# Performance work log

Hardware: AMD Instinct MI355X
Metric: run time of the kernel (lower is better)

Reference implementation:

```python
import jax, jax.numpy as jnp
import numpy as np

N, E, F_IN, HID, L_EXTRA, G = 50000, 800000, 128, 128, 3, 256

def gcn_conv(x, W, b, src, dst, norm):
    # PyG GCNConv: out = D^-1/2 (A+I) D^-1/2 (X W) + b  (self-loops included in src/dst)
    xw = x @ W                                  # [N, out]
    msg = xw[src] * norm[:, None]               # [E+N, out]
    return jax.ops.segment_sum(msg, dst, num_segments=N) + b

def setup_inputs() -> dict:
    key = jax.random.key(0)
    ks = jax.random.split(key, 12)
    x = jax.random.normal(ks[0], (N, F_IN), dtype=jnp.float32)
    edge_index = jax.random.randint(ks[1], (2, E), 0, N, dtype=jnp.int64)
    batch = jnp.sort(jax.random.randint(ks[2], (N,), 0, G, dtype=jnp.int64))
    s = 1.0 / np.sqrt(HID)
    W0 = jax.random.uniform(ks[3], (F_IN, HID), jnp.float32, -s, s)
    b0 = jnp.zeros((HID,), jnp.float32)
    Wh = jax.random.uniform(ks[4], (L_EXTRA, HID, HID), jnp.float32, -s, s)
    bh = jnp.zeros((L_EXTRA, HID), jnp.float32)
    s1 = 1.0 / np.sqrt(3 * HID)
    lin1_w = jax.random.uniform(ks[5], (3 * HID, HID), jnp.float32, -s1, s1)
    lin1_b = jax.random.uniform(ks[6], (HID,), jnp.float32, -s1, s1)
    s2 = 1.0 / np.sqrt(HID)
    lin2_w = jax.random.uniform(ks[7], (HID, 2), jnp.float32, -s2, s2)
    lin2_b = jax.random.uniform(ks[8], (2,), jnp.float32, -s2, s2)
    return {"x": x, "edge_index": edge_index, "batch": batch,
            "W0": W0, "b0": b0, "Wh": Wh, "bh": bh,
            "lin1_w": lin1_w, "lin1_b": lin1_b, "lin2_w": lin2_w, "lin2_b": lin2_b}

def reference(x, edge_index, batch, W0, b0, Wh, bh, lin1_w, lin1_b, lin2_w, lin2_b):
    # add self-loops once (shared by all layers)
    loop = jnp.arange(N, dtype=edge_index.dtype)
    src = jnp.concatenate([edge_index[0], loop])
    dst = jnp.concatenate([edge_index[1], loop])
    deg = jax.ops.segment_sum(jnp.ones_like(dst, dtype=x.dtype), dst, num_segments=N)
    dinv = jnp.where(deg > 0, jax.lax.rsqrt(deg), 0.0)
    norm = dinv[src] * dinv[dst]                # [E+N]

    h = jax.nn.relu(gcn_conv(x, W0, b0, src, dst, norm))
    for i in range(L_EXTRA):
        h = jax.nn.relu(gcn_conv(h, Wh[i], bh[i], src, dst, norm))

    # multi-pool over graphs in the batch
    p_sum = jax.ops.segment_sum(h, batch, num_segments=G)
    cnt = jax.ops.segment_sum(jnp.ones((N,), h.dtype), batch, num_segments=G)
    p_mean = p_sum / jnp.maximum(cnt, 1.0)[:, None]
    p_max = jax.ops.segment_max(h, batch, num_segments=G)
    p_max = jnp.where(jnp.isfinite(p_max), p_max, 0.0)  # guard empty graphs
    g = jnp.concatenate([p_sum, p_mean, p_max], axis=1)  # [G, 3*HID]

    g = jax.nn.relu(g @ lin1_w + lin1_b)        # dropout p=0.5 is identity in eval
    logits = g @ lin2_w + lin2_b
    return jax.nn.log_softmax(logits, axis=-1)
```

## Files before the change

kernel.cpp:

```cpp
#include <hip/hip_runtime.h>
#include <hip/hip_fp16.h>
#include <cstddef>

typedef _Float16 f16x8 __attribute__((ext_vector_type(8)));
typedef float f32x4 __attribute__((ext_vector_type(4)));
typedef unsigned short ushort8 __attribute__((ext_vector_type(8)));


__global__ __launch_bounds__(256) void k_bhist(const int* __restrict__ dst, int* __restrict__ bcnt, int e) {
    __shared__ int lh[256];
    int t = threadIdx.x;
    lh[t] = 0;
    __syncthreads();
    for (int i = blockIdx.x * 256 + t; i < e; i += gridDim.x * 256)
        atomicAdd(&lh[dst[i] >> 8], 1);
    __syncthreads();
    if (lh[t] > 0) atomicAdd(&bcnt[t], lh[t]);
}

__global__ __launch_bounds__(256) void k_bscan(const int* __restrict__ bcnt, int* __restrict__ bebase,
                                               int* __restrict__ bcbase, int* __restrict__ bcur,
                                               int* __restrict__ rowptr, int nbk, int n, int e) {
    __shared__ int se[256], sc[256];
    int t = threadIdx.x;
    int ec = (t < nbk) ? bcnt[t] : 0;
    int nodes = 0;
    if (t < nbk) {
        nodes = n - t * 256;
        if (nodes > 256) nodes = 256;
        if (nodes < 0) nodes = 0;
    }
    se[t] = ec;
    sc[t] = ec + nodes;
    __syncthreads();
    for (int off = 1; off < 256; off <<= 1) {
        int ve = (t >= off) ? se[t - off] : 0;
        int vc = (t >= off) ? sc[t - off] : 0;
        __syncthreads();
        se[t] += ve;
        sc[t] += vc;
        __syncthreads();
    }
    if (t < nbk) {
        bebase[t] = se[t] - ec;
        bcbase[t] = sc[t] - (ec + nodes);
        bcur[t]   = se[t] - ec;
    }
    if (t == 0) {
        bebase[nbk] = e;
        rowptr[n] = e + n;
    }
}

__global__ __launch_bounds__(256) void k_bscatter(const int* __restrict__ src, const int* __restrict__ dst,
                                                  int* __restrict__ bcur, int* __restrict__ bedges, int e) {
    __shared__ int lh[256];
    __shared__ int gbase[256];
    int t = threadIdx.x;
    lh[t] = 0;
    __syncthreads();
    int base = blockIdx.x * 4096;
    int s_[16], d_[16];
#pragma unroll
    for (int u = 0; u < 16; ++u) {
        int j = base + u * 256 + t;
        if (j < e) {
            s_[u] = src[j];
            d_[u] = dst[j];
            atomicAdd(&lh[d_[u] >> 8], 1);
        } else {
            d_[u] = -1;
        }
    }
    __syncthreads();
    if (lh[t] > 0) gbase[t] = atomicAdd(&bcur[t], lh[t]);
    __syncthreads();
    lh[t] = 0;
    __syncthreads();
#pragma unroll
    for (int u = 0; u < 16; ++u) {
        if (d_[u] >= 0) {
            int bk = d_[u] >> 8;
            int lpos = atomicAdd(&lh[bk], 1);
            bedges[gbase[bk] + lpos] = (s_[u] << 8) | (d_[u] & 255);
        }
    }
}

__global__ __launch_bounds__(256) void k_bcsr(const int* __restrict__ bedges, const int* __restrict__ bebase,
                                              const int* __restrict__ bcbase, int* __restrict__ rowptr,
                                              float* __restrict__ dinv, int* __restrict__ csr_s, int n) {
    __shared__ int lh[256], lcur[256];
    int b = blockIdx.x, t = threadIdx.x;
    int n0 = b << 8;
    int nb = n - n0; if (nb > 256) nb = 256;
    int e0 = bebase[b], e1 = bebase[b + 1];
    int cb = bcbase[b];
    lh[t] = 0;
    __syncthreads();
    for (int i = e0 + t; i < e1; i += 256)
        atomicAdd(&lh[bedges[i] & 255], 1);
    __syncthreads();
    int deg = (t < nb) ? (lh[t] + 1) : 0;
    __syncthreads();
    lh[t] = deg;
    __syncthreads();
    for (int off = 1; off < 256; off <<= 1) {
        int v = (t >= off) ? lh[t - off] : 0;
        __syncthreads();
        lh[t] += v;
        __syncthreads();
    }
    int lrp = lh[t] - deg;
    if (t < nb) {
        rowptr[n0 + t] = cb + lrp;
        dinv[n0 + t] = rsqrtf((float)deg);
    }
    lcur[t] = lrp;
    __syncthreads();
    for (int i = e0 + t; i < e1; i += 256) {
        int ed = bedges[i];
        int pos = cb + atomicAdd(&lcur[ed & 255], 1);
        csr_s[pos] = (int)((unsigned)ed >> 8);
    }
    if (t < nb) {
        int pos = cb + atomicAdd(&lcur[t], 1);
        csr_s[pos] = n0 + t;
    }
}

__global__ __launch_bounds__(256) void k_wprep(const float* __restrict__ W0, const float* __restrict__ Wh,
                                               __half* __restrict__ WP, int* __restrict__ bcnt, int nlayers) {
    int layer = blockIdx.x;
    int t = threadIdx.x;
    if (layer >= nlayers) {
        bcnt[t] = 0;
        return;
    }
    const float* W = (layer == 0) ? W0 : Wh + (size_t)(layer - 1) * 16384;
    __half* out = WP + (size_t)layer * 16384;
    for (int u = 0; u < 64; ++u) {
        int o = u * 256 + t;
        int i  = o & 7;
        int l  = (o >> 3) & 63;
        int kc = (o >> 9) & 3;
        int nt = o >> 11;
        int k   = kc * 32 + ((l >> 4) << 3) + i;
        int col = nt * 16 + (l & 15);
        out[o] = __float2half(W[k * 128 + col]);
    }
}

__global__ __launch_bounds__(256) void k_gemm(const __half* __restrict__ H, const __half* __restrict__ WP,
                                              const float* __restrict__ dinv, __half* __restrict__ O,
                                              int n) {
    __shared__ __half wl[16384];
    const int t = threadIdx.x;
#pragma unroll
    for (int u = 0; u < 8; ++u) {
        int idx = (u * 256 + t) * 8;
        *(ushort8*)&wl[idx] = *(const ushort8*)&WP[idx];
    }
    const int wid = t >> 6, l = t & 63;
    const int row0 = blockIdx.x * 128 + wid * 32;
    const int ar = l & 15, g = l >> 4;

    f16x8 a[2][4];
    float dv[2][4];
#pragma unroll
    for (int mt = 0; mt < 2; ++mt) {
        int row = row0 + mt * 16 + ar;
        int rc = min(row, n - 1);
#pragma unroll
        for (int kc = 0; kc < 4; ++kc)
            a[mt][kc] = *(const f16x8*)&H[(size_t)rc * 128 + kc * 32 + g * 8];
#pragma unroll
        for (int r = 0; r < 4; ++r) {
            int orow = row0 + mt * 16 + g * 4 + r;
            dv[mt][r] = dinv[min(orow, n - 1)];
        }
    }
    __syncthreads();

#pragma unroll
    for (int nt = 0; nt < 8; ++nt) {
        f16x8 b[4];
#pragma unroll
        for (int kc = 0; kc < 4; ++kc)
            b[kc] = *(f16x8*)&wl[((nt * 4 + kc) * 64 + l) * 8];
#pragma unroll
        for (int mt = 0; mt < 2; ++mt) {
            f32x4 acc = {0.f, 0.f, 0.f, 0.f};
#pragma unroll
            for (int kc = 0; kc < 4; ++kc)
                acc = __builtin_amdgcn_mfma_f32_16x16x32_f16(a[mt][kc], b[kc], acc, 0, 0, 0);
#pragma unroll
            for (int r = 0; r < 4; ++r) {
                int orow = row0 + mt * 16 + g * 4 + r;
                if (orow < n)
                    O[(size_t)orow * 128 + nt * 16 + ar] = __float2half(acc[r] * dv[mt][r]);
            }
        }
    }
}

__global__ __launch_bounds__(256) void k_gemm32(const float* __restrict__ H, const __half* __restrict__ WP,
                                                const float* __restrict__ dinv, __half* __restrict__ O,
                                                int n) {
    __shared__ __half wl[16384];
    const int t = threadIdx.x;
#pragma unroll
    for (int u = 0; u < 8; ++u) {
        int idx = (u * 256 + t) * 8;
        *(ushort8*)&wl[idx] = *(const ushort8*)&WP[idx];
    }
    const int wid = t >> 6, l = t & 63;
    const int row0 = blockIdx.x * 128 + wid * 32;
    const int ar = l & 15, g = l >> 4;

    f16x8 a[2][4];
    float dv[2][4];
#pragma unroll
    for (int mt = 0; mt < 2; ++mt) {
        int row = row0 + mt * 16 + ar;
        int rc = min(row, n - 1);
#pragma unroll
        for (int kc = 0; kc < 4; ++kc) {
            float4 p0 = *(const float4*)&H[(size_t)rc * 128 + kc * 32 + g * 8];
            float4 p1 = *(const float4*)&H[(size_t)rc * 128 + kc * 32 + g * 8 + 4];
            f16x8 av;
            av[0] = (_Float16)p0.x; av[1] = (_Float16)p0.y; av[2] = (_Float16)p0.z; av[3] = (_Float16)p0.w;
            av[4] = (_Float16)p1.x; av[5] = (_Float16)p1.y; av[6] = (_Float16)p1.z; av[7] = (_Float16)p1.w;
            a[mt][kc] = av;
        }
#pragma unroll
        for (int r = 0; r < 4; ++r) {
            int orow = row0 + mt * 16 + g * 4 + r;
            dv[mt][r] = dinv[min(orow, n - 1)];
        }
    }
    __syncthreads();

#pragma unroll
    for (int nt = 0; nt < 8; ++nt) {
        f16x8 b[4];
#pragma unroll
        for (int kc = 0; kc < 4; ++kc)
            b[kc] = *(f16x8*)&wl[((nt * 4 + kc) * 64 + l) * 8];
#pragma unroll
        for (int mt = 0; mt < 2; ++mt) {
            f32x4 acc = {0.f, 0.f, 0.f, 0.f};
#pragma unroll
            for (int kc = 0; kc < 4; ++kc)
                acc = __builtin_amdgcn_mfma_f32_16x16x32_f16(a[mt][kc], b[kc], acc, 0, 0, 0);
#pragma unroll
            for (int r = 0; r < 4; ++r) {
                int orow = row0 + mt * 16 + g * 4 + r;
                if (orow < n)
                    O[(size_t)orow * 128 + nt * 16 + ar] = __float2half(acc[r] * dv[mt][r]);
            }
        }
    }
}

__global__ __launch_bounds__(256) void k_agg(const __half* __restrict__ XW, const int* __restrict__ cs,
                                             const int* __restrict__ rp, const float* __restrict__ dinv,
                                             const float* __restrict__ bias, __half* __restrict__ Hn, int n) {
    int wid  = (blockIdx.x * 256 + threadIdx.x) >> 6;
    int lane = threadIdx.x & 63;
    if (wid >= n) return;
    int s = rp[wid], e = rp[wid + 1];
    const int g = lane >> 4, fs = lane & 15;
    float acc0[8], acc1[8];
#pragma unroll
    for (int k = 0; k < 8; ++k) { acc0[k] = 0.f; acc1[k] = 0.f; }
    for (int base = s; base < e; base += 64) {
        int m = e - base;
        if (m > 64) m = 64;
        int myi = (lane < m) ? cs[base + lane] : 0;
#pragma unroll 2
        for (int j = 0; j < m; j += 8) {
            int ia = __shfl(myi, j + g);
            int ib = __shfl(myi, j + 4 + g);
            if (j + g < m) {
                f16x8 va = *(const f16x8*)&XW[(size_t)ia * 128 + fs * 8];
#pragma unroll
                for (int k = 0; k < 8; ++k) acc0[k] += (float)va[k];
            }
            if (j + 4 + g < m) {
                f16x8 vb = *(const f16x8*)&XW[(size_t)ib * 128 + fs * 8];
#pragma unroll
                for (int k = 0; k < 8; ++k) acc1[k] += (float)vb[k];
            }
        }
    }
#pragma unroll
    for (int k = 0; k < 8; ++k) acc0[k] += acc1[k];
#pragma unroll
    for (int k = 0; k < 8; ++k) acc0[k] += __shfl_xor(acc0[k], 16);
#pragma unroll
    for (int k = 0; k < 8; ++k) acc0[k] += __shfl_xor(acc0[k], 32);
    if (g == 0) {
        float dvv = dinv[wid];
        float4 bb0 = *(const float4*)&bias[fs * 8];
        float4 bb1 = *(const float4*)&bias[fs * 8 + 4];
        float bb[8] = {bb0.x, bb0.y, bb0.z, bb0.w, bb1.x, bb1.y, bb1.z, bb1.w};
        f16x8 o;
#pragma unroll
        for (int k = 0; k < 8; ++k)
            o[k] = (_Float16)fmaxf(fmaf(acc0[k], dvv, bb[k]), 0.f);
        *(f16x8*)&Hn[(size_t)wid * 128 + fs * 8] = o;
    }
}

__global__ __launch_bounds__(256) void k_poolhead(const __half* __restrict__ H, const int* __restrict__ batch,
                                                  const float* __restrict__ w1, const float* __restrict__ b1,
                                                  const float* __restrict__ w2, const float* __restrict__ b2,
                                                  float* __restrict__ out, int n) {
    __shared__ float lsum[16][128];
    __shared__ float lmax[16][128];
    __shared__ float gv[384];
    __shared__ float o1[128];
    __shared__ int bnd[2];
    int g = blockIdx.x, t = threadIdx.x;
    if (t < 2) {
        int key = g + t;
        int lo = 0, hi = n;
        while (lo < hi) {
            int mid = (lo + hi) >> 1;
            if (batch[mid] < key) lo = mid + 1; else hi = mid;
        }
        bnd[t] = lo;
    }
    __syncthreads();
    const int s = bnd[0], e = bnd[1];
    const int rg = t >> 4, fb = t & 15;
    float sum8[8], max8[8];
#pragma unroll
    for (int j = 0; j < 8; ++j) { sum8[j] = 0.f; max8[j] = 0.f; }
    for (int r = s + rg; r < e; r += 16) {
        f16x8 v = *(const f16x8*)&H[(size_t)r * 128 + fb * 8];
#pragma unroll
        for (int j = 0; j < 8; ++j) {
            float x = (float)v[j];
            sum8[j] += x;
            max8[j] = fmaxf(max8[j], x);
        }
    }
#pragma unroll
    for (int j = 0; j < 8; ++j) {
        lsum[rg][fb * 8 + j] = sum8[j];
        lmax[rg][fb * 8 + j] = max8[j];
    }
    __syncthreads();
    if (t < 128) {
        float sum = 0.f, mx = 0.f;
#pragma unroll
        for (int r = 0; r < 16; ++r) {
            sum += lsum[r][t];
            mx = fmaxf(mx, lmax[r][t]);
        }
        float cnt = (float)(e - s);
        gv[t]       = sum;
        gv[128 + t] = sum / fmaxf(cnt, 1.f);
        gv[256 + t] = mx;
    }
    __syncthreads();
    if (t < 128) {
        float acc = b1[t];
#pragma unroll 8
        for (int k = 0; k < 384; ++k) acc = fmaf(gv[k], w1[k * 128 + t], acc);
        o1[t] = fmaxf(acc, 0.f);
    }
    __syncthreads();
    if (t < 64) {
        float p0 = o1[t] * w2[t * 2 + 0] + o1[t + 64] * w2[(t + 64) * 2 + 0];
        float p1 = o1[t] * w2[t * 2 + 1] + o1[t + 64] * w2[(t + 64) * 2 + 1];
        for (int off = 32; off > 0; off >>= 1) {
            p0 += __shfl_down(p0, off);
            p1 += __shfl_down(p1, off);
        }
        if (t == 0) {
            float l0 = p0 + b2[0], l1 = p1 + b2[1];
            float m = fmaxf(l0, l1);
            float lse = m + logf(expf(l0 - m) + expf(l1 - m));
            out[g * 2 + 0] = l0 - lse;
            out[g * 2 + 1] = l1 - lse;
        }
    }
}


extern "C" void kernel_launch(void* const* d_in, const int* in_sizes, int n_in,
                              void* d_out, int out_size, void* d_ws, size_t ws_size,
                              hipStream_t stream) {
    const float* x     = (const float*)d_in[0];
    const int*   ei    = (const int*)d_in[1];
    const int*   batch = (const int*)d_in[2];
    const float* W0    = (const float*)d_in[3];
    const float* b0    = (const float*)d_in[4];
    const float* Wh    = (const float*)d_in[5];
    const float* bh    = (const float*)d_in[6];
    const float* l1w   = (const float*)d_in[7];
    const float* l1b   = (const float*)d_in[8];
    const float* l2w   = (const float*)d_in[9];
    const float* l2b   = (const float*)d_in[10];
    float* out = (float*)d_out;

    const int N  = in_sizes[0] / 128;
    const int E  = in_sizes[1] / 2;
    const int G  = out_size / 2;
    const int LX = in_sizes[5] / (128 * 128);
    const int NB = (N + 255) / 256;

    const int* src = ei;
    const int* dst = ei + E;

    char* p = (char*)d_ws;
    auto alloc = [&](size_t bytes) -> void* {
        void* r = (void*)p;
        p += (bytes + 255) & ~(size_t)255;
        return r;
    };
    int*    rowptr = (int*)alloc((size_t)(N + 1) * 4);
    float*  dinv   = (float*)alloc((size_t)N * 4);
    int*    bcnt   = (int*)alloc(1040);
    int*    bebase = (int*)alloc(1040);
    int*    bcbase = (int*)alloc(1040);
    int*    bcur   = (int*)alloc(1040);
    int*    csr_s  = (int*)alloc((size_t)(E + N) * 4);
    int*    bedges = (int*)alloc((size_t)E * 4);
    __half* h16    = (__half*)alloc((size_t)N * 128 * 2);
    __half* xw16   = (__half*)alloc((size_t)N * 128 * 2);
    __half* wp     = (__half*)alloc((size_t)(LX + 1) * 16384 * 2);

    k_wprep<<<LX + 2, 256, 0, stream>>>(W0, Wh, wp, bcnt, LX + 1);

    k_bhist<<<NB, 256, 0, stream>>>(dst, bcnt, E);
    k_bscan<<<1, 256, 0, stream>>>(bcnt, bebase, bcbase, bcur, rowptr, NB, N, E);
    k_bscatter<<<(E + 4095) / 4096, 256, 0, stream>>>(src, dst, bcur, bedges, E);
    k_bcsr<<<NB, 256, 0, stream>>>(bedges, bebase, bcbase, rowptr, dinv, csr_s, N);

    const int gemmBlocks = (N + 127) / 128;
    const int aggBlocks  = (N + 3) / 4;

    k_gemm32<<<gemmBlocks, 256, 0, stream>>>(x, wp, dinv, xw16, N);
    k_agg<<<aggBlocks, 256, 0, stream>>>(xw16, csr_s, rowptr, dinv, b0, h16, N);
    for (int l = 0; l < LX; ++l) {
        k_gemm<<<gemmBlocks, 256, 0, stream>>>(h16, wp + (size_t)(l + 1) * 16384, dinv, xw16, N);
        k_agg<<<aggBlocks, 256, 0, stream>>>(xw16, csr_s, rowptr, dinv, bh + (size_t)l * 128, h16, N);
    }

    k_poolhead<<<G, 256, 0, stream>>>(h16, batch, l1w, l1b, l2w, l2b, out, N);
}
```

Baseline: 249.5 us.

## Store features in four 32-column planes and aggregate per plane for cache locality

Feature matrices move from row-major [N,128] to four planar [N,32] chunks, and the aggregation kernel now runs a separate block range per chunk. Each chunk of the gathered table is about 3.2 MB, so the random neighbour gathers in one pass should stay in L2 instead of sweeping the full 12.8 MB table. The cost is four times as many waves, each rereading the CSR indices and rowptr, plus 64-byte gather segments instead of 256-byte rows. The GEMM and pooling kernels are updated to read and write the planar layout.

```diff
diff --git a/kernel.cpp b/kernel.cpp
--- a/kernel.cpp
+++ b/kernel.cpp
@@ -164,6 +164,7 @@
     const int wid = t >> 6, l = t & 63;
     const int row0 = blockIdx.x * 128 + wid * 32;
     const int ar = l & 15, g = l >> 4;
+    const size_t pn = (size_t)n * 32;
 
     f16x8 a[2][4];
     float dv[2][4];
@@ -173,7 +174,7 @@
         int rc = min(row, n - 1);
 #pragma unroll
         for (int kc = 0; kc < 4; ++kc)
-            a[mt][kc] = *(const f16x8*)&H[(size_t)rc * 128 + kc * 32 + g * 8];
+            a[mt][kc] = *(const f16x8*)&H[pn * kc + (size_t)rc * 32 + g * 8];
 #pragma unroll
         for (int r = 0; r < 4; ++r) {
             int orow = row0 + mt * 16 + g * 4 + r;
@@ -198,7 +199,8 @@
             for (int r = 0; r < 4; ++r) {
                 int orow = row0 + mt * 16 + g * 4 + r;
                 if (orow < n)
-                    O[(size_t)orow * 128 + nt * 16 + ar] = __float2half(acc[r] * dv[mt][r]);
+                    O[pn * (nt >> 1) + (size_t)orow * 32 + (nt & 1) * 16 + ar] =
+                        __float2half(acc[r] * dv[mt][r]);
             }
         }
     }
@@ -217,6 +219,7 @@
     const int wid = t >> 6, l = t & 63;
     const int row0 = blockIdx.x * 128 + wid * 32;
     const int ar = l & 15, g = l >> 4;
+    const size_t pn = (size_t)n * 32;
 
     f16x8 a[2][4];
     float dv[2][4];
@@ -257,59 +260,62 @@
             for (int r = 0; r < 4; ++r) {
                 int orow = row0 + mt * 16 + g * 4 + r;
                 if (orow < n)
-                    O[(size_t)orow * 128 + nt * 16 + ar] = __float2half(acc[r] * dv[mt][r]);
+                    O[pn * (nt >> 1) + (size_t)orow * 32 + (nt & 1) * 16 + ar] =
+                        __float2half(acc[r] * dv[mt][r]);
             }
         }
     }
 }
 
-__global__ __launch_bounds__(256) void k_agg(const __half* __restrict__ XW, const int* __restrict__ cs,
-                                             const int* __restrict__ rp, const float* __restrict__ dinv,
-                                             const float* __restrict__ bias, __half* __restrict__ Hn, int n) {
-    int wid  = (blockIdx.x * 256 + threadIdx.x) >> 6;
+__global__ __launch_bounds__(256) void k_aggc(const __half* __restrict__ XWp, const int* __restrict__ cs,
+                                              const int* __restrict__ rp, const float* __restrict__ dinv,
+                                              const float* __restrict__ bias, __half* __restrict__ Hp,
+                                              int n, int bpc) {
+    int c   = blockIdx.x / bpc;
+    int nb  = blockIdx.x - c * bpc;
+    int wid = (nb * 256 + threadIdx.x) >> 6;
     int lane = threadIdx.x & 63;
     if (wid >= n) return;
+    const size_t pn = (size_t)n * 32;
+    const __half* P = XWp + pn * c;
     int s = rp[wid], e = rp[wid + 1];
-    const int g = lane >> 4, fs = lane & 15;
-    float acc0[8], acc1[8];
-#pragma unroll
-    for (int k = 0; k < 8; ++k) { acc0[k] = 0.f; acc1[k] = 0.f; }
+    const int g4 = lane >> 2, q = lane & 3;
+    float acc[8];
+#pragma unroll
+    for (int k = 0; k < 8; ++k) acc[k] = 0.f;
     for (int base = s; base < e; base += 64) {
         int m = e - base;
         if (m > 64) m = 64;
         int myi = (lane < m) ? cs[base + lane] : 0;
 #pragma unroll 2
-        for (int j = 0; j < m; j += 8) {
-            int ia = __shfl(myi, j + g);
-            int ib = __shfl(myi, j + 4 + g);
-            if (j + g < m) {
-                f16x8 va = *(const f16x8*)&XW[(size_t)ia * 128 + fs * 8];
-#pragma unroll
-                for (int k = 0; k < 8; ++k) acc0[k] += (float)va[k];
+        for (int j = 0; j < m; j += 16) {
+            int r = j + g4;
+            int idx = __shfl(myi, r);
+            if (r < m) {
+                f16x8 v = *(const f16x8*)&P[(size_t)idx * 32 + q * 8];
+#pragma unroll
+                for (int k = 0; k < 8; ++k) acc[k] += (float)v[k];
             }
-            if (j + 4 + g < m) {
-                f16x8 vb = *(const f16x8*)&XW[(size_t)ib * 128 + fs * 8];
-#pragma unroll
-                for (int k = 0; k < 8; ++k) acc1[k] += (float)vb[k];
-            }
-        }
-    }
-#pragma unroll
-    for (int k = 0; k < 8; ++k) acc0[k] += acc1[k];
-#pragma unroll
-    for (int k = 0; k < 8; ++k) acc0[k] += __shfl_xor(acc0[k], 16);
-#pragma unroll
-    for (int k = 0; k < 8; ++k) acc0[k] += __shfl_xor(acc0[k], 32);
-    if (g == 0) {
+        }
+    }
+#pragma unroll
+    for (int k = 0; k < 8; ++k) acc[k] += __shfl_xor(acc[k], 4);
+#pragma unroll
+    for (int k = 0; k < 8; ++k) acc[k] += __shfl_xor(acc[k], 8);
+#pragma unroll
+    for (int k = 0; k < 8; ++k) acc[k] += __shfl_xor(acc[k], 16);
+#pragma unroll
+    for (int k = 0; k < 8; ++k) acc[k] += __shfl_xor(acc[k], 32);
+    if (g4 == 0) {
         float dvv = dinv[wid];
-        float4 bb0 = *(const float4*)&bias[fs * 8];
-        float4 bb1 = *(const float4*)&bias[fs * 8 + 4];
+        float4 bb0 = *(const float4*)&bias[c * 32 + q * 8];
+        float4 bb1 = *(const float4*)&bias[c * 32 + q * 8 + 4];
         float bb[8] = {bb0.x, bb0.y, bb0.z, bb0.w, bb1.x, bb1.y, bb1.z, bb1.w};
         f16x8 o;
 #pragma unroll
         for (int k = 0; k < 8; ++k)
-            o[k] = (_Float16)fmaxf(fmaf(acc0[k], dvv, bb[k]), 0.f);
-        *(f16x8*)&Hn[(size_t)wid * 128 + fs * 8] = o;
+            o[k] = (_Float16)fmaxf(fmaf(acc[k], dvv, bb[k]), 0.f);
+        *(f16x8*)&Hp[pn * c + (size_t)wid * 32 + q * 8] = o;
     }
 }
 
@@ -335,11 +341,14 @@
     __syncthreads();
     const int s = bnd[0], e = bnd[1];
     const int rg = t >> 4, fb = t & 15;
+    const size_t pn = (size_t)n * 32;
+    const __half* Hc = H + pn * (fb >> 2);
+    const int fo = (fb & 3) * 8;
     float sum8[8], max8[8];
 #pragma unroll
     for (int j = 0; j < 8; ++j) { sum8[j] = 0.f; max8[j] = 0.f; }
     for (int r = s + rg; r < e; r += 16) {
-        f16x8 v = *(const f16x8*)&H[(size_t)r * 128 + fb * 8];
+        f16x8 v = *(const f16x8*)&Hc[(size_t)r * 32 + fo];
 #pragma unroll
         for (int j = 0; j < 8; ++j) {
             float x = (float)v[j];
@@ -442,13 +451,13 @@
     k_bcsr<<<NB, 256, 0, stream>>>(bedges, bebase, bcbase, rowptr, dinv, csr_s, N);
 
     const int gemmBlocks = (N + 127) / 128;
-    const int aggBlocks  = (N + 3) / 4;
+    const int bpc        = (N + 3) / 4;
 
     k_gemm32<<<gemmBlocks, 256, 0, stream>>>(x, wp, dinv, xw16, N);
-    k_agg<<<aggBlocks, 256, 0, stream>>>(xw16, csr_s, rowptr, dinv, b0, h16, N);
+    k_aggc<<<4 * bpc, 256, 0, stream>>>(xw16, csr_s, rowptr, dinv, b0, h16, N, bpc);
     for (int l = 0; l < LX; ++l) {
         k_gemm<<<gemmBlocks, 256, 0, stream>>>(h16, wp + (size_t)(l + 1) * 16384, dinv, xw16, N);
-        k_agg<<<aggBlocks, 256, 0, stream>>>(xw16, csr_s, rowptr, dinv, bh + (size_t)l * 128, h16, N);
+        k_aggc<<<4 * bpc, 256, 0, stream>>>(xw16, csr_s, rowptr, dinv, bh + (size_t)l * 128, h16, N, bpc);
     }
 
     k_poolhead<<<G, 256, 0, stream>>>(h16, batch, l1w, l1b, l2w, l2b, out, N);
```

Result: slower. 411.1 us (+64.8%).

## Merge setup kernels and overlap first-layer GEMM with CSR build

Applied to the files above, without the earlier changes.

Weight packing is folded into the degree-histogram kernel, and the bucket-to-CSR build shares one launch with the first-layer GEMM. Because that GEMM can no longer wait for dinv, it skips the source-side scaling, and the first aggregation applies dinv per gathered source row instead. The aggregation inner loop is also fully unrolled with an early break. This removes launches and lets independent work overlap, at the cost of an extra dinv gather per edge in layer one.

```diff
diff --git a/kernel.cpp b/kernel.cpp
--- a/kernel.cpp
+++ b/kernel.cpp
@@ -6,16 +6,35 @@
 typedef float f32x4 __attribute__((ext_vector_type(4)));
 typedef unsigned short ushort8 __attribute__((ext_vector_type(8)));
 
-
-__global__ __launch_bounds__(256) void k_bhist(const int* __restrict__ dst, int* __restrict__ bcnt, int e) {
+__global__ __launch_bounds__(256) void k_setup1(const float* __restrict__ W0, const float* __restrict__ Wh,
+                                                __half* __restrict__ WP, int nlayers,
+                                                const int* __restrict__ dst, int* __restrict__ bcnt,
+                                                int e, int nb) {
     __shared__ int lh[256];
     int t = threadIdx.x;
-    lh[t] = 0;
-    __syncthreads();
-    for (int i = blockIdx.x * 256 + t; i < e; i += gridDim.x * 256)
-        atomicAdd(&lh[dst[i] >> 8], 1);
-    __syncthreads();
-    if (lh[t] > 0) atomicAdd(&bcnt[t], lh[t]);
+    if ((int)blockIdx.x < nlayers) {
+        int layer = blockIdx.x;
+        const float* W = (layer == 0) ? W0 : Wh + (size_t)(layer - 1) * 16384;
+        __half* out = WP + (size_t)layer * 16384;
+        for (int u = 0; u < 64; ++u) {
+            int o = u * 256 + t;
+            int i  = o & 7;
+            int l  = (o >> 3) & 63;
+            int kc = (o >> 9) & 3;
+            int nt = o >> 11;
+            int k   = kc * 32 + ((l >> 4) << 3) + i;
+            int col = nt * 16 + (l & 15);
+            out[o] = __float2half(W[k * 128 + col]);
+        }
+    } else {
+        int bi = blockIdx.x - nlayers;
+        lh[t] = 0;
+        __syncthreads();
+        for (int i = bi * 256 + t; i < e; i += nb * 256)
+            atomicAdd(&lh[dst[i] >> 8], 1);
+        __syncthreads();
+        if (lh[t] > 0) atomicAdd(&bcnt[t], lh[t]);
+    }
 }
 
 __global__ __launch_bounds__(256) void k_bscan(const int* __restrict__ bcnt, int* __restrict__ bebase,
@@ -87,67 +106,100 @@
     }
 }
 
-__global__ __launch_bounds__(256) void k_bcsr(const int* __restrict__ bedges, const int* __restrict__ bebase,
-                                              const int* __restrict__ bcbase, int* __restrict__ rowptr,
-                                              float* __restrict__ dinv, int* __restrict__ csr_s, int n) {
-    __shared__ int lh[256], lcur[256];
-    int b = blockIdx.x, t = threadIdx.x;
-    int n0 = b << 8;
-    int nb = n - n0; if (nb > 256) nb = 256;
-    int e0 = bebase[b], e1 = bebase[b + 1];
-    int cb = bcbase[b];
-    lh[t] = 0;
-    __syncthreads();
-    for (int i = e0 + t; i < e1; i += 256)
-        atomicAdd(&lh[bedges[i] & 255], 1);
-    __syncthreads();
-    int deg = (t < nb) ? (lh[t] + 1) : 0;
-    __syncthreads();
-    lh[t] = deg;
-    __syncthreads();
-    for (int off = 1; off < 256; off <<= 1) {
-        int v = (t >= off) ? lh[t - off] : 0;
-        __syncthreads();
-        lh[t] += v;
-        __syncthreads();
-    }
-    int lrp = lh[t] - deg;
-    if (t < nb) {
-        rowptr[n0 + t] = cb + lrp;
-        dinv[n0 + t] = rsqrtf((float)deg);
-    }
-    lcur[t] = lrp;
-    __syncthreads();
-    for (int i = e0 + t; i < e1; i += 256) {
-        int ed = bedges[i];
-        int pos = cb + atomicAdd(&lcur[ed & 255], 1);
-        csr_s[pos] = (int)((unsigned)ed >> 8);
-    }
-    if (t < nb) {
-        int pos = cb + atomicAdd(&lcur[t], 1);
-        csr_s[pos] = n0 + t;
-    }
-}
-
-__global__ __launch_bounds__(256) void k_wprep(const float* __restrict__ W0, const float* __restrict__ Wh,
-                                               __half* __restrict__ WP, int* __restrict__ bcnt, int nlayers) {
-    int layer = blockIdx.x;
-    int t = threadIdx.x;
-    if (layer >= nlayers) {
-        bcnt[t] = 0;
-        return;
-    }
-    const float* W = (layer == 0) ? W0 : Wh + (size_t)(layer - 1) * 16384;
-    __half* out = WP + (size_t)layer * 16384;
-    for (int u = 0; u < 64; ++u) {
-        int o = u * 256 + t;
-        int i  = o & 7;
-        int l  = (o >> 3) & 63;
-        int kc = (o >> 9) & 3;
-        int nt = o >> 11;
-        int k   = kc * 32 + ((l >> 4) << 3) + i;
-        int col = nt * 16 + (l & 15);
-        out[o] = __float2half(W[k * 128 + col]);
+__global__ __launch_bounds__(256) void k_mix(const int* __restrict__ bedges, const int* __restrict__ bebase,
+                                             const int* __restrict__ bcbase, int* __restrict__ rowptr,
+                                             float* __restrict__ dinv, int* __restrict__ csr_s, int n,
+                                             const float* __restrict__ X, const __half* __restrict__ WP,
+                                             __half* __restrict__ O, int nbk) {
+    __shared__ __half wl[16384];
+    const int t = threadIdx.x;
+    if ((int)blockIdx.x < nbk) {
+        int* lh   = (int*)wl;
+        int* lcur = lh + 256;
+        int b = blockIdx.x;
+        int n0 = b << 8;
+        int nb = n - n0; if (nb > 256) nb = 256;
+        int e0 = bebase[b], e1 = bebase[b + 1];
+        int cb = bcbase[b];
+        lh[t] = 0;
+        __syncthreads();
+        for (int i = e0 + t; i < e1; i += 256)
+            atomicAdd(&lh[bedges[i] & 255], 1);
+        __syncthreads();
+        int deg = (t < nb) ? (lh[t] + 1) : 0;
+        __syncthreads();
+        lh[t] = deg;
+        __syncthreads();
+        for (int off = 1; off < 256; off <<= 1) {
+            int v = (t >= off) ? lh[t - off] : 0;
+            __syncthreads();
+            lh[t] += v;
+            __syncthreads();
+        }
+        int lrp = lh[t] - deg;
+        if (t < nb) {
+            rowptr[n0 + t] = cb + lrp;
+            dinv[n0 + t] = rsqrtf((float)deg);
+        }
+        lcur[t] = lrp;
+        __syncthreads();
+        for (int i = e0 + t; i < e1; i += 256) {
+            int ed = bedges[i];
+            int pos = cb + atomicAdd(&lcur[ed & 255], 1);
+            csr_s[pos] = (int)((unsigned)ed >> 8);
+        }
+        if (t < nb) {
+            int pos = cb + atomicAdd(&lcur[t], 1);
+            csr_s[pos] = n0 + t;
+        }
+    } else {
+#pragma unroll
+        for (int u = 0; u < 8; ++u) {
+            int idx = (u * 256 + t) * 8;
+            *(ushort8*)&wl[idx] = *(const ushort8*)&WP[idx];
+        }
+        const int gb = blockIdx.x - nbk;
+        const int wid = t >> 6, l = t & 63;
+        const int row0 = gb * 128 + wid * 32;
+        const int ar = l & 15, g = l >> 4;
+
+        f16x8 a[2][4];
+#pragma unroll
+        for (int mt = 0; mt < 2; ++mt) {
+            int row = row0 + mt * 16 + ar;
+            int rc = min(row, n - 1);
+#pragma unroll
+            for (int kc = 0; kc < 4; ++kc) {
+                float4 p0 = *(const float4*)&X[(size_t)rc * 128 + kc * 32 + g * 8];
+                float4 p1 = *(const float4*)&X[(size_t)rc * 128 + kc * 32 + g * 8 + 4];
+                f16x8 av;
+                av[0] = (_Float16)p0.x; av[1] = (_Float16)p0.y; av[2] = (_Float16)p0.z; av[3] = (_Float16)p0.w;
+                av[4] = (_Float16)p1.x; av[5] = (_Float16)p1.y; av[6] = (_Float16)p1.z; av[7] = (_Float16)p1.w;
+                a[mt][kc] = av;
+            }
+        }
+        __syncthreads();
+
+#pragma unroll
+        for (int nt = 0; nt < 8; ++nt) {
+            f16x8 b[4];
+#pragma unroll
+            for (int kc = 0; kc < 4; ++kc)
+                b[kc] = *(f16x8*)&wl[((nt * 4 + kc) * 64 + l) * 8];
+#pragma unroll
+            for (int mt = 0; mt < 2; ++mt) {
+                f32x4 acc = {0.f, 0.f, 0.f, 0.f};
+#pragma unroll
+                for (int kc = 0; kc < 4; ++kc)
+                    acc = __builtin_amdgcn_mfma_f32_16x16x32_f16(a[mt][kc], b[kc], acc, 0, 0, 0);
+#pragma unroll
+                for (int r = 0; r < 4; ++r) {
+                    int orow = row0 + mt * 16 + g * 4 + r;
+                    if (orow < n)
+                        O[(size_t)orow * 128 + nt * 16 + ar] = __float2half(acc[r]);
+                }
+            }
+        }
     }
 }
 
@@ -204,65 +256,7 @@
     }
 }
 
-__global__ __launch_bounds__(256) void k_gemm32(const float* __restrict__ H, const __half* __restrict__ WP,
-                                                const float* __restrict__ dinv, __half* __restrict__ O,
-                                                int n) {
-    __shared__ __half wl[16384];
-    const int t = threadIdx.x;
-#pragma unroll
-    for (int u = 0; u < 8; ++u) {
-        int idx = (u * 256 + t) * 8;
-        *(ushort8*)&wl[idx] = *(const ushort8*)&WP[idx];
-    }
-    const int wid = t >> 6, l = t & 63;
-    const int row0 = blockIdx.x * 128 + wid * 32;
-    const int ar = l & 15, g = l >> 4;
-
-    f16x8 a[2][4];
-    float dv[2][4];
-#pragma unroll
-    for (int mt = 0; mt < 2; ++mt) {
-        int row = row0 + mt * 16 + ar;
-        int rc = min(row, n - 1);
-#pragma unroll
-        for (int kc = 0; kc < 4; ++kc) {
-            float4 p0 = *(const float4*)&H[(size_t)rc * 128 + kc * 32 + g * 8];
-            float4 p1 = *(const float4*)&H[(size_t)rc * 128 + kc * 32 + g * 8 + 4];
-            f16x8 av;
-            av[0] = (_Float16)p0.x; av[1] = (_Float16)p0.y; av[2] = (_Float16)p0.z; av[3] = (_Float16)p0.w;
-            av[4] = (_Float16)p1.x; av[5] = (_Float16)p1.y; av[6] = (_Float16)p1.z; av[7] = (_Float16)p1.w;
-            a[mt][kc] = av;
-        }
-#pragma unroll
-        for (int r = 0; r < 4; ++r) {
-            int orow = row0 + mt * 16 + g * 4 + r;
-            dv[mt][r] = dinv[min(orow, n - 1)];
-        }
-    }
-    __syncthreads();
-
-#pragma unroll
-    for (int nt = 0; nt < 8; ++nt) {
-        f16x8 b[4];
-#pragma unroll
-        for (int kc = 0; kc < 4; ++kc)
-            b[kc] = *(f16x8*)&wl[((nt * 4 + kc) * 64 + l) * 8];
-#pragma unroll
-        for (int mt = 0; mt < 2; ++mt) {
-            f32x4 acc = {0.f, 0.f, 0.f, 0.f};
-#pragma unroll
-            for (int kc = 0; kc < 4; ++kc)
-                acc = __builtin_amdgcn_mfma_f32_16x16x32_f16(a[mt][kc], b[kc], acc, 0, 0, 0);
-#pragma unroll
-            for (int r = 0; r < 4; ++r) {
-                int orow = row0 + mt * 16 + g * 4 + r;
-                if (orow < n)
-                    O[(size_t)orow * 128 + nt * 16 + ar] = __float2half(acc[r] * dv[mt][r]);
-            }
-        }
-    }
-}
-
+template <int SCALE_SRC>
 __global__ __launch_bounds__(256) void k_agg(const __half* __restrict__ XW, const int* __restrict__ cs,
                                              const int* __restrict__ rp, const float* __restrict__ dinv,
                                              const float* __restrict__ bias, __half* __restrict__ Hn, int n) {
@@ -278,19 +272,25 @@
         int m = e - base;
         if (m > 64) m = 64;
         int myi = (lane < m) ? cs[base + lane] : 0;
-#pragma unroll 2
-        for (int j = 0; j < m; j += 8) {
+#pragma unroll
+        for (int jj = 0; jj < 8; ++jj) {
+            const int j = jj * 8;
+            if (j >= m) break;
             int ia = __shfl(myi, j + g);
             int ib = __shfl(myi, j + 4 + g);
             if (j + g < m) {
                 f16x8 va = *(const f16x8*)&XW[(size_t)ia * 128 + fs * 8];
-#pragma unroll
-                for (int k = 0; k < 8; ++k) acc0[k] += (float)va[k];
+                float wsa = SCALE_SRC ? dinv[ia] : 1.f;
+#pragma unroll
+                for (int k = 0; k < 8; ++k)
+                    acc0[k] = SCALE_SRC ? fmaf(wsa, (float)va[k], acc0[k]) : (acc0[k] + (float)va[k]);
             }
             if (j + 4 + g < m) {
                 f16x8 vb = *(const f16x8*)&XW[(size_t)ib * 128 + fs * 8];
-#pragma unroll
-                for (int k = 0; k < 8; ++k) acc1[k] += (float)vb[k];
+                float wsb = SCALE_SRC ? dinv[ib] : 1.f;
+#pragma unroll
+                for (int k = 0; k < 8; ++k)
+                    acc1[k] = SCALE_SRC ? fmaf(wsb, (float)vb[k], acc1[k]) : (acc1[k] + (float)vb[k]);
             }
         }
     }
@@ -434,21 +434,20 @@
     __half* xw16   = (__half*)alloc((size_t)N * 128 * 2);
     __half* wp     = (__half*)alloc((size_t)(LX + 1) * 16384 * 2);
 
-    k_wprep<<<LX + 2, 256, 0, stream>>>(W0, Wh, wp, bcnt, LX + 1);
-
-    k_bhist<<<NB, 256, 0, stream>>>(dst, bcnt, E);
+    const int gemmBlocks = (N + 127) / 128;
+    const int aggBlocks  = (N + 3) / 4;
+
+    hipMemsetAsync(bcnt, 0, 1024, stream);
+    k_setup1<<<(LX + 1) + NB, 256, 0, stream>>>(W0, Wh, wp, LX + 1, dst, bcnt, E, NB);
     k_bscan<<<1, 256, 0, stream>>>(bcnt, bebase, bcbase, bcur, rowptr, NB, N, E);
     k_bscatter<<<(E + 4095) / 4096, 256, 0, stream>>>(src, dst, bcur, bedges, E);
-    k_bcsr<<<NB, 256, 0, stream>>>(bedges, bebase, bcbase, rowptr, dinv, csr_s, N);
-
-    const int gemmBlocks = (N + 127) / 128;
-    const int aggBlocks  = (N + 3) / 4;
-
-    k_gemm32<<<gemmBlocks, 256, 0, stream>>>(x, wp, dinv, xw16, N);
-    k_agg<<<aggBlocks, 256, 0, stream>>>(xw16, csr_s, rowptr, dinv, b0, h16, N);
+    k_mix<<<NB + gemmBlocks, 256, 0, stream>>>(bedges, bebase, bcbase, rowptr, dinv, csr_s, N,
+                                               x, wp, xw16, NB);
+
+    k_agg<1><<<aggBlocks, 256, 0, stream>>>(xw16, csr_s, rowptr, dinv, b0, h16, N);
     for (int l = 0; l < LX; ++l) {
         k_gemm<<<gemmBlocks, 256, 0, stream>>>(h16, wp + (size_t)(l + 1) * 16384, dinv, xw16, N);
-        k_agg<<<aggBlocks, 256, 0, stream>>>(xw16, csr_s, rowptr, dinv, bh + (size_t)l * 128, h16, N);
+        k_agg<0><<<aggBlocks, 256, 0, stream>>>(xw16, csr_s, rowptr, dinv, bh + (size_t)l * 128, h16, N);
     }
 
     k_poolhead<<<G, 256, 0, stream>>>(h16, batch, l1w, l1b, l2w, l2b, out, N);
```

New measurement: 242.8 us. 1.03x faster.
